# Kernel optimization log

Hardware: AMD Instinct MI355X
Metric: run time of the kernel (lower is better)

The kernel has to match this reference:

```python
import jax, jax.numpy as jnp
import numpy as np

TEMPERATURE = 0.5


def _nt_xent(emb_i, emb_j, temperature):
    n = emb_i.shape[0]
    reps = jnp.concatenate([emb_i, emb_j], axis=0)  # [2N, D]
    # cosine similarity via normalized GEMM (same math as broadcasted F.cosine_similarity)
    eps = 1e-8
    norms = jnp.maximum(jnp.linalg.norm(reps, axis=1, keepdims=True), eps)
    z = reps / norms
    sim = z @ z.T  # [2N, 2N]
    # positives: sim[k, k+N] for k<N and sim[k, k-N] for k>=N
    sim_ij = jnp.diagonal(sim, offset=n)
    sim_ji = jnp.diagonal(sim, offset=-n)
    positives = jnp.concatenate([sim_ij, sim_ji], axis=0)  # [2N]
    logits = sim / temperature
    # mask out self-similarity (diagonal) in denominator
    neg_mask = 1.0 - jnp.eye(2 * n, dtype=logits.dtype)
    denom = jnp.sum(neg_mask * jnp.exp(logits), axis=1)  # [2N]
    loss_partial = -(positives / temperature - jnp.log(denom))
    return jnp.sum(loss_partial) / (2 * n)


def setup_inputs() -> dict:
    key = jax.random.key(0)
    k1, k2 = jax.random.split(key)
    N, D = 4096, 256
    emb_i = jax.random.normal(k1, (N, D), dtype=jnp.float32)
    emb_j = jax.random.normal(k2, (N, D), dtype=jnp.float32)
    return {"emb_i": emb_i, "emb_j": emb_j}


def reference(emb_i, emb_j):
    return _nt_xent(emb_i, emb_j, TEMPERATURE)
```

## Files before the change

### kernel.cpp

```cpp
#include <hip/hip_runtime.h>
#include <hip/hip_bf16.h>
#include <math.h>

#define D      256
#define N2     8192
#define NHALF  4096
#define TILE   128
#define BK     64
#define NCH    4
#define LDW    68
#define NBLK2  4096
#define TPB    512

typedef __bf16 bf16x8_t __attribute__((ext_vector_type(8)));
typedef __bf16 bf16x4_t __attribute__((ext_vector_type(4)));
typedef float  f32x4_t  __attribute__((ext_vector_type(4)));

__global__ __launch_bounds__(256) void prep_kernel(const float* __restrict__ a,
                                                   const float* __restrict__ b,
                                                   __bf16* __restrict__ zb,
                                                   float* __restrict__ g_pos,
                                                   float* __restrict__ g_denom,
                                                   unsigned* __restrict__ g_t1) {
    const int tid = threadIdx.x;
    const int gt  = blockIdx.x * 256 + tid;
    if (gt < N2) g_denom[gt] = 0.0f;
    if (gt < 64 * 32 + 1) g_t1[gt] = 0u;

    const int w = blockIdx.x * 4 + (tid >> 6);
    const int l = tid & 63;
    float4 x = ((const float4*)(a + (size_t)w * D))[l];
    float4 y = ((const float4*)(b + (size_t)w * D))[l];
    float sxx = x.x * x.x + x.y * x.y + x.z * x.z + x.w * x.w;
    float syy = y.x * y.x + y.y * y.y + y.z * y.z + y.w * y.w;
    float sxy = x.x * y.x + x.y * y.y + x.z * y.z + x.w * y.w;
    #pragma unroll
    for (int off = 32; off; off >>= 1) {
        sxx += __shfl_xor(sxx, off, 64);
        syy += __shfl_xor(syy, off, 64);
        sxy += __shfl_xor(sxy, off, 64);
    }
    const float rx = 1.0f / fmaxf(sqrtf(sxx), 1e-8f);
    const float ry = 1.0f / fmaxf(sqrtf(syy), 1e-8f);

    bf16x4_t ox, oy;
    ox[0] = (__bf16)(x.x * rx); ox[1] = (__bf16)(x.y * rx);
    ox[2] = (__bf16)(x.z * rx); ox[3] = (__bf16)(x.w * rx);
    oy[0] = (__bf16)(y.x * ry); oy[1] = (__bf16)(y.y * ry);
    oy[2] = (__bf16)(y.z * ry); oy[3] = (__bf16)(y.w * ry);
    *(bf16x4_t*)(zb + (size_t)w * D + l * 4)           = ox;
    *(bf16x4_t*)(zb + (size_t)(w + NHALF) * D + l * 4) = oy;

    if (l == 0) {
        const float p = sxy * rx * ry;
        g_pos[w]         = p;
        g_pos[w + NHALF] = p;
    }
}

__global__ __launch_bounds__(TPB, 4) void sim_kernel(const __bf16* __restrict__ zb,
                                                     float* __restrict__ g_denom,
                                                     const float* __restrict__ g_pos,
                                                     unsigned* __restrict__ g_t1,
                                                     float* __restrict__ out) {
    __shared__ __bf16 ldsA[2][TILE * LDW];
    __shared__ __bf16 ldsB[2][TILE * LDW];
    __shared__ float  sw[8];
    __shared__ bool   amLast;

    const int tid    = threadIdx.x;
    const int l      = tid & 63;
    const int lane15 = l & 15;
    const int quad   = l >> 4;
    const int w      = tid >> 6;
    const int wr     = (w & 3) * 32;
    const int wc     = (w >> 2) * 64;

    const int bi = blockIdx.x >> 6;
    const int bj = blockIdx.x & 63;

    const int r = tid >> 2;
    const int q = tid & 3;
    const __bf16* ga = zb + (size_t)(bi * TILE + r) * D + q * 16;
    const __bf16* gb = zb + (size_t)(bj * TILE + r) * D + q * 16;
    const int wofs = r * LDW + q * 16;

    bf16x8_t sa0, sa1, sb0, sb1;
    auto load_regs = [&](int c) {
        const int k0 = c * BK;
        sa0 = *(const bf16x8_t*)(ga + k0);
        sa1 = *(const bf16x8_t*)(ga + k0 + 8);
        sb0 = *(const bf16x8_t*)(gb + k0);
        sb1 = *(const bf16x8_t*)(gb + k0 + 8);
    };
    auto write_lds = [&](int buf) {
        *(bf16x8_t*)(&ldsA[buf][wofs])     = sa0;
        *(bf16x8_t*)(&ldsA[buf][wofs + 8]) = sa1;
        *(bf16x8_t*)(&ldsB[buf][wofs])     = sb0;
        *(bf16x8_t*)(&ldsB[buf][wofs + 8]) = sb1;
    };

    f32x4_t acc[2][4];
    #pragma unroll
    for (int mi = 0; mi < 2; ++mi)
        #pragma unroll
        for (int nj = 0; nj < 4; ++nj)
            acc[mi][nj] = (f32x4_t){0.f, 0.f, 0.f, 0.f};

    auto compute = [&](int buf) {
        #pragma unroll
        for (int ks = 0; ks < 2; ++ks) {
            bf16x8_t af[2], bff[4];
            #pragma unroll
            for (int mi = 0; mi < 2; ++mi)
                af[mi] = *(const bf16x8_t*)(&ldsA[buf][(wr + mi * 16 + lane15) * LDW + ks * 32 + quad * 8]);
            #pragma unroll
            for (int nj = 0; nj < 4; ++nj)
                bff[nj] = *(const bf16x8_t*)(&ldsB[buf][(wc + nj * 16 + lane15) * LDW + ks * 32 + quad * 8]);
            #pragma unroll
            for (int mi = 0; mi < 2; ++mi)
                #pragma unroll
                for (int nj = 0; nj < 4; ++nj)
                    acc[mi][nj] = __builtin_amdgcn_mfma_f32_16x16x32_bf16(bff[nj], af[mi], acc[mi][nj], 0, 0, 0);
        }
    };

    load_regs(0);
    write_lds(0);
    __syncthreads();

    int cur = 0;
    #pragma unroll
    for (int c = 0; c < NCH; ++c) {
        if (c + 1 < NCH) load_regs(c + 1);
        compute(cur);
        if (c + 1 < NCH) {
            write_lds(cur ^ 1);
            __syncthreads();
            cur ^= 1;
        }
    }

    float rs[2] = {0.f, 0.f};
    #pragma unroll
    for (int mi = 0; mi < 2; ++mi) {
        #pragma unroll
        for (int nj = 0; nj < 4; ++nj) {
            const bool dn = (bi == bj) && (wr + mi * 16 == wc + nj * 16);
            #pragma unroll
            for (int t = 0; t < 4; ++t) {
                float e = exp2f(acc[mi][nj][t] * 2.8853900817779268f);
                if (dn && (quad * 4 + t) == lane15) e = 0.0f;
                rs[mi] += e;
            }
        }
    }
    #pragma unroll
    for (int mi = 0; mi < 2; ++mi) {
        rs[mi] += __shfl_xor(rs[mi], 16, 64);
        rs[mi] += __shfl_xor(rs[mi], 32, 64);
    }
    if (l < 16) {
        #pragma unroll
        for (int mi = 0; mi < 2; ++mi)
            atomicAdd(&g_denom[bi * TILE + wr + mi * 16 + l], rs[mi]);
    }

    __syncthreads();
    if (tid == 0) {
        asm volatile("s_waitcnt vmcnt(0)" ::: "memory");
        unsigned t1 = __hip_atomic_fetch_add(&g_t1[bi * 32], 1u, __ATOMIC_RELAXED,
                                             __HIP_MEMORY_SCOPE_AGENT);
        bool grpLast = (t1 == 63);
        unsigned t2 = 0;
        if (grpLast)
            t2 = __hip_atomic_fetch_add(&g_t1[64 * 32], 1u, __ATOMIC_RELAXED,
                                        __HIP_MEMORY_SCOPE_AGENT);
        amLast = grpLast && (t2 == 63);
    }
    __syncthreads();
    if (!amLast) return;

    float local = 0.0f;
    for (int k = tid; k < N2; k += TPB) {
        float dn = __hip_atomic_load(&g_denom[k], __ATOMIC_RELAXED,
                                     __HIP_MEMORY_SCOPE_AGENT);
        local += logf(dn) - 2.0f * g_pos[k];
    }
    #pragma unroll
    for (int off = 32; off; off >>= 1) local += __shfl_xor(local, off, 64);
    if (l == 0) sw[w] = local;
    __syncthreads();
    if (tid == 0) {
        float s = 0.f;
        #pragma unroll
        for (int i = 0; i < 8; ++i) s += sw[i];
        out[0] = s / (float)N2;
    }
}

extern "C" void kernel_launch(void* const* d_in, const int* in_sizes, int n_in,
                              void* d_out, int out_size, void* d_ws, size_t ws_size,
                              hipStream_t stream) {
    const float* emb_i = (const float*)d_in[0];
    const float* emb_j = (const float*)d_in[1];

    __bf16*   zb      = (__bf16*)d_ws;
    float*    g_denom = (float*)((char*)d_ws + (size_t)N2 * D * 2);
    float*    g_pos   = g_denom + N2;
    unsigned* g_t1    = (unsigned*)(g_pos + N2);
    float*    out     = (float*)d_out;

    prep_kernel<<<NHALF / 4, 256, 0, stream>>>(emb_i, emb_j, zb, g_pos, g_denom, g_t1);
    sim_kernel<<<NBLK2, TPB, 0, stream>>>(zb, g_denom, g_pos, g_t1, out);
}
```

Measured before the change: 122.3 us.

## Exploit similarity-matrix symmetry by computing only upper-triangular tiles

The similarity GEMM is now launched only over the upper-triangular block tiles (2080 instead of 4096). Each off-diagonal tile also reduces its exp values along columns and atomically adds them to the denominators of the transposed rows. This roughly halves the MFMA and exp work. In exchange it adds per-tile column shuffles and extra global atomics, plus float-sqrt index decoding and reworked completion counters.

```diff
diff --git a/kernel.cpp b/kernel.cpp
--- a/kernel.cpp
+++ b/kernel.cpp
@@ -9,7 +9,7 @@
 #define BK     64
 #define NCH    4
 #define LDW    68
-#define NBLK2  4096
+#define NTRI   2080
 #define TPB    512
 
 typedef __bf16 bf16x8_t __attribute__((ext_vector_type(8)));
@@ -25,7 +25,7 @@
     const int tid = threadIdx.x;
     const int gt  = blockIdx.x * 256 + tid;
     if (gt < N2) g_denom[gt] = 0.0f;
-    if (gt < 64 * 32 + 1) g_t1[gt] = 0u;
+    if (gt < 65 * 32 + 1) g_t1[gt] = 0u;
 
     const int w = blockIdx.x * 4 + (tid >> 6);
     const int l = tid & 63;
@@ -76,8 +76,12 @@
     const int wr     = (w & 3) * 32;
     const int wc     = (w >> 2) * 64;
 
-    const int bi = blockIdx.x >> 6;
-    const int bj = blockIdx.x & 63;
+    const int k = blockIdx.x;
+    int bi = (int)(64.5f - sqrtf(64.5f * 64.5f - 2.0f * (float)k));
+    while ((bi * (129 - bi)) / 2 > k) --bi;
+    while (((bi + 1) * (128 - bi)) / 2 <= k) ++bi;
+    const int bj   = bi + (k - (bi * (129 - bi)) / 2);
+    const bool diag = (bi == bj);
 
     const int r = tid >> 2;
     const int q = tid & 3;
@@ -142,16 +146,23 @@
     }
 
     float rs[2] = {0.f, 0.f};
+    float cp[4][4];
+    #pragma unroll
+    for (int nj = 0; nj < 4; ++nj)
+        #pragma unroll
+        for (int t = 0; t < 4; ++t) cp[nj][t] = 0.f;
+
     #pragma unroll
     for (int mi = 0; mi < 2; ++mi) {
         #pragma unroll
         for (int nj = 0; nj < 4; ++nj) {
-            const bool dn = (bi == bj) && (wr + mi * 16 == wc + nj * 16);
+            const bool dn = diag && (wr + mi * 16 == wc + nj * 16);
             #pragma unroll
             for (int t = 0; t < 4; ++t) {
                 float e = exp2f(acc[mi][nj][t] * 2.8853900817779268f);
                 if (dn && (quad * 4 + t) == lane15) e = 0.0f;
                 rs[mi] += e;
+                cp[nj][t] += e;
             }
         }
     }
@@ -165,27 +176,45 @@
         for (int mi = 0; mi < 2; ++mi)
             atomicAdd(&g_denom[bi * TILE + wr + mi * 16 + l], rs[mi]);
     }
+    if (!diag) {
+        #pragma unroll
+        for (int nj = 0; nj < 4; ++nj)
+            #pragma unroll
+            for (int t = 0; t < 4; ++t) {
+                cp[nj][t] += __shfl_xor(cp[nj][t], 1, 64);
+                cp[nj][t] += __shfl_xor(cp[nj][t], 2, 64);
+                cp[nj][t] += __shfl_xor(cp[nj][t], 4, 64);
+                cp[nj][t] += __shfl_xor(cp[nj][t], 8, 64);
+            }
+        if (lane15 == 0) {
+            #pragma unroll
+            for (int nj = 0; nj < 4; ++nj)
+                #pragma unroll
+                for (int t = 0; t < 4; ++t)
+                    atomicAdd(&g_denom[bj * TILE + wc + nj * 16 + quad * 4 + t], cp[nj][t]);
+        }
+    }
 
     __syncthreads();
     if (tid == 0) {
         asm volatile("s_waitcnt vmcnt(0)" ::: "memory");
-        unsigned t1 = __hip_atomic_fetch_add(&g_t1[bi * 32], 1u, __ATOMIC_RELAXED,
-                                             __HIP_MEMORY_SCOPE_AGENT);
-        bool grpLast = (t1 == 63);
+        unsigned t1 = __hip_atomic_fetch_add(&g_t1[(blockIdx.x >> 5) * 32], 1u,
+                                             __ATOMIC_RELAXED, __HIP_MEMORY_SCOPE_AGENT);
+        bool grpLast = (t1 == 31);
         unsigned t2 = 0;
         if (grpLast)
-            t2 = __hip_atomic_fetch_add(&g_t1[64 * 32], 1u, __ATOMIC_RELAXED,
+            t2 = __hip_atomic_fetch_add(&g_t1[65 * 32], 1u, __ATOMIC_RELAXED,
                                         __HIP_MEMORY_SCOPE_AGENT);
-        amLast = grpLast && (t2 == 63);
+        amLast = grpLast && (t2 == 64);
     }
     __syncthreads();
     if (!amLast) return;
 
     float local = 0.0f;
-    for (int k = tid; k < N2; k += TPB) {
-        float dn = __hip_atomic_load(&g_denom[k], __ATOMIC_RELAXED,
+    for (int kk = tid; kk < N2; kk += TPB) {
+        float dn = __hip_atomic_load(&g_denom[kk], __ATOMIC_RELAXED,
                                      __HIP_MEMORY_SCOPE_AGENT);
-        local += logf(dn) - 2.0f * g_pos[k];
+        local += logf(dn) - 2.0f * g_pos[kk];
     }
     #pragma unroll
     for (int off = 32; off; off >>= 1) local += __shfl_xor(local, off, 64);
@@ -212,5 +241,5 @@
     float*    out     = (float*)d_out;
 
     prep_kernel<<<NHALF / 4, 256, 0, stream>>>(emb_i, emb_j, zb, g_pos, g_denom, g_t1);
-    sim_kernel<<<NBLK2, TPB, 0, stream>>>(zb, g_denom, g_pos, g_t1, out);
+    sim_kernel<<<NTRI, TPB, 0, stream>>>(zb, g_denom, g_pos, g_t1, out);
 }
```

New measurement: 115.6 us. 5.5% less time.
